# Performance work log

Measured on AMD Instinct MI355X. Metric: run time of the kernel, lower is better.

## Reference

```python
import jax, jax.numpy as jnp
import numpy as np

N, C, H, W = 32, 49, 9, 9   # batch, spectral bands (=outplane), spatial patch
MSIZE, K, PAD = 24, 7, 3    # conv3d out channels, spectral kernel, padding
EPS = 1e-5


def setup_inputs() -> dict:
    key = jax.random.key(0)
    k1, k2, k3 = jax.random.split(key, 3)
    x = jax.random.normal(k1, (N, C, H, W), dtype=jnp.float32)
    # Conv3d(1, MSIZE, [7,1,1]) params, PyTorch default uniform init
    fan_in = 1 * K * 1 * 1
    bound = 1.0 / np.sqrt(fan_in)
    conv_w = jax.random.uniform(k2, (MSIZE, 1, K, 1, 1), jnp.float32, -bound, bound)
    conv_b = jax.random.uniform(k3, (MSIZE,), jnp.float32, -bound, bound)
    # BatchNorm2d(49) affine params at init
    gamma = jnp.ones((C,), jnp.float32)
    beta = jnp.zeros((C,), jnp.float32)
    return {"x": x, "conv_w": conv_w, "conv_b": conv_b, "gamma": gamma, "beta": beta}


def reference(x, conv_w, conv_b, gamma, beta):
    n, c, h, w = x.shape
    # Conv3d over (depth=spectral, h, w) with kernel [K,1,1]: depth preserved
    x5 = x[:, None]  # (n,1,c,h,w)
    m = jax.lax.conv_general_dilated(
        x5, conv_w, window_strides=(1, 1, 1),
        padding=[(PAD, PAD), (0, 0), (0, 0)],
        dimension_numbers=("NCDHW", "OIDHW", "NCDHW"),
    ) + conv_b[None, :, None, None, None]        # (n, MSIZE, c, h, w)
    d = m.shape[1] * m.shape[2]                   # d = MSIZE * c
    mask = jax.nn.softmax(m.reshape(n, d, h * w), axis=-1).reshape(n, d, h, w)
    # original computes convm0 twice -> mask1 == mask0; reuse `mask` for both
    fk = jnp.einsum("ndhw,nchw->ncd", mask, x)    # (n, c, d)
    # out[n,c,h,w] = sum_d leaky_relu(fk[n,c,d] * mask[n,d,h,w])
    big = jnp.einsum("ncd,ndhw->ncdhw", fk, mask)  # (n,c,d,h,w) large intermediate
    out = jax.nn.leaky_relu(big, negative_slope=0.01).sum(axis=2)
    out = out + x                                  # residual
    # BatchNorm2d in training mode: batch statistics over (n,h,w) per channel
    mean = out.mean(axis=(0, 2, 3))
    var = out.var(axis=(0, 2, 3))
    out = (out - mean[:, None, None]) * jax.lax.rsqrt(var[:, None, None] + EPS)
    out = out * gamma[:, None, None] + beta[:, None, None]
    return out
```

## Files before the change

kernel.cpp:

```cpp
#include <hip/hip_runtime.h>
#include <hip/hip_bf16.h>

#define NN    32
#define CC    49
#define HWSZ  81
#define MSZ   24
#define KSZ   7
#define PADSZ 3
#define NHW   (NN*HWSZ)
#define NCHW  (NN*CC*HWSZ)

#define XSB_S  104
#define MSK_S  104
#define MSKT_S 72
#define G_S    72

typedef __attribute__((ext_vector_type(8))) short short8;
typedef __attribute__((ext_vector_type(4))) short short4v;
typedef __attribute__((ext_vector_type(4))) float f32x4;

__device__ __forceinline__ short f2b(float v) {
    unsigned u = __float_as_uint(v);
    u += 0x7fffu + ((u >> 16) & 1u);
    return (short)(u >> 16);
}
__device__ __forceinline__ float b2f(short s) {
    return __uint_as_float(((unsigned)(unsigned short)s) << 16);
}

__global__ __launch_bounds__(256) void fuse_k1(
    const float* __restrict__ x, const float* __restrict__ cw,
    const float* __restrict__ cb, float* __restrict__ acc, int use_ws)
{
    __shared__ short xsb [64 * XSB_S];
    __shared__ short msk [64 * MSK_S];
    __shared__ short mskT[96 * MSKT_S];
    __shared__ short gm  [64 * G_S];

    const int o = blockIdx.x;
    const int n = blockIdx.y;
    const int t = threadIdx.x;
    const int lane = t & 63;
    const int wv = t >> 6;
    const int lr = lane & 15;
    const int lq = lane >> 4;

    const float* xg = x + (size_t)n * CC * HWSZ;
    float wk[KSZ];
    #pragma unroll
    for (int k = 0; k < KSZ; ++k) wk[k] = cw[o * KSZ + k];
    const float bias = cb[o];

    const f32x4 z4 = {0.f, 0.f, 0.f, 0.f};
    for (int i = t; i < CC * HWSZ; i += 256) {
        int c = i / HWSZ, hw = i - c * HWSZ;
        xsb[c * XSB_S + hw] = f2b(xg[i]);
    }
    if (t < CC) {
        short* row = xsb + t * XSB_S;
        #pragma unroll
        for (int cq = 81; cq < 88; ++cq) row[cq] = 0;
        *(f32x4*)(row + 88) = z4;
        *(f32x4*)(row + 96) = z4;
    }
    for (int j = t; j < 15 * 13; j += 256) {
        int rr = j / 13, cg = j - rr * 13;
        *(f32x4*)(xsb + (49 + rr) * XSB_S + cg * 8) = z4;
    }
    for (int i = t; i < 832; i += 256) ((f32x4*)msk)[i] = z4;
    for (int i = t; i < 864; i += 256) ((f32x4*)mskT)[i] = z4;
    __syncthreads();

    #pragma unroll
    for (int it = 0; it < 4; ++it) {
        int dd = it * 16 + wv * 4 + lq;
        if (dd < CC) {
            float a0 = 0.f, a1 = 0.f, a2 = 0.f, a3 = 0.f, a4 = 0.f, a5 = 0.f;
            #pragma unroll
            for (int k = 0; k < KSZ; ++k) {
                int r = dd + k - PADSZ;
                if (r >= 0 && r < CC) {
                    const short* xr = xsb + r * XSB_S;
                    short4v xa = *(const short4v*)(xr + 4 * lr);
                    float w = wk[k];
                    a0 += w * b2f(xa[0]);
                    a1 += w * b2f(xa[1]);
                    a2 += w * b2f(xa[2]);
                    a3 += w * b2f(xa[3]);
                    a4 += w * b2f(xr[64 + lr]);
                    if (lr == 0) a5 += w * b2f(xr[80]);
                }
            }
            float e0 = __expf(a0 + bias), e1 = __expf(a1 + bias);
            float e2 = __expf(a2 + bias), e3 = __expf(a3 + bias);
            float e4 = __expf(a4 + bias);
            float e5 = (lr == 0) ? __expf(a5 + bias) : 0.f;
            float s = ((e0 + e1) + (e2 + e3)) + (e4 + e5);
            #pragma unroll
            for (int off = 8; off; off >>= 1) s += __shfl_xor(s, off, 64);
            float inv = __builtin_amdgcn_rcpf(s);
            short4v pk;
            pk[0] = f2b(e0 * inv); pk[1] = f2b(e1 * inv);
            pk[2] = f2b(e2 * inv); pk[3] = f2b(e3 * inv);
            short b4 = f2b(e4 * inv);
            short* mrow = msk + dd * MSK_S;
            *(short4v*)(mrow + 4 * lr) = pk;
            mrow[64 + lr] = b4;
            mskT[(4 * lr    ) * MSKT_S + dd] = pk[0];
            mskT[(4 * lr + 1) * MSKT_S + dd] = pk[1];
            mskT[(4 * lr + 2) * MSKT_S + dd] = pk[2];
            mskT[(4 * lr + 3) * MSKT_S + dd] = pk[3];
            mskT[(64 + lr   ) * MSKT_S + dd] = b4;
            if (lr == 0) {
                short b5 = f2b(e5 * inv);
                mrow[80] = b5;
                mskT[80 * MSKT_S + dd] = b5;
            }
        }
    }
    __syncthreads();

    {
        short8 a2[3];
        #pragma unroll
        for (int ks = 0; ks < 3; ++ks)
            a2[ks] = *(const short8*)&msk[(wv * 16 + lr) * MSK_S + ks * 32 + lq * 8];
        #pragma unroll
        for (int nt = 0; nt < 4; ++nt) {
            f32x4 accv = {0.f, 0.f, 0.f, 0.f};
            #pragma unroll
            for (int ks = 0; ks < 3; ++ks) {
                short8 b = *(const short8*)&xsb[(nt * 16 + lr) * XSB_S + ks * 32 + lq * 8];
                accv = __builtin_amdgcn_mfma_f32_16x16x32_bf16(a2[ks], b, accv, 0, 0, 0);
            }
            short4v pk;
            #pragma unroll
            for (int r = 0; r < 4; ++r) {
                float v = accv[r];
                v = (v >= 0.f) ? v : 0.01f * v;
                pk[r] = f2b(v);
            }
            *(short4v*)&gm[(nt * 16 + lr) * G_S + wv * 16 + lq * 4] = pk;
        }
    }
    __syncthreads();

    {
        short* bws = (short*)acc + (size_t)(o * NN + n) * CC * HWSZ;
        float* dstn = acc + (size_t)n * CC * HWSZ;
        short8 a1[2];
        #pragma unroll
        for (int ks = 0; ks < 2; ++ks)
            a1[ks] = *(const short8*)&gm[(wv * 16 + lr) * G_S + ks * 32 + lq * 8];
        #pragma unroll
        for (int nt = 0; nt < 6; ++nt) {
            f32x4 accv = {0.f, 0.f, 0.f, 0.f};
            #pragma unroll
            for (int ks = 0; ks < 2; ++ks) {
                short8 b = *(const short8*)&mskT[(nt * 16 + lr) * MSKT_S + ks * 32 + lq * 8];
                accv = __builtin_amdgcn_mfma_f32_16x16x32_bf16(a1[ks], b, accv, 0, 0, 0);
            }
            int hw = nt * 16 + lr;
            if (hw < HWSZ) {
                int cb = wv * 16 + lq * 4;
                if (use_ws) {
                    #pragma unroll
                    for (int r = 0; r < 4; ++r) {
                        int c = cb + r;
                        if (c < CC) bws[c * HWSZ + hw] = f2b(accv[r]);
                    }
                } else {
                    #pragma unroll
                    for (int r = 0; r < 4; ++r) {
                        int c = cb + r;
                        if (c < CC) atomicAdd(dstn + c * HWSZ + hw, accv[r]);
                    }
                }
            }
        }
    }
}

__global__ __launch_bounds__(1024) void fuse_k2w(
    const short* __restrict__ bws, const float* __restrict__ x,
    const float* __restrict__ gamma, const float* __restrict__ beta,
    float* __restrict__ out)
{
    const int c = blockIdx.x;
    const int t = threadIdx.x;
    float vals[3];
    float sum = 0.f, sq = 0.f;
    int cnt = 0;
    for (int i = t; i < NHW; i += 1024) {
        int n = i / HWSZ;
        int hw = i - n * HWSZ;
        int idx = (n * CC + c) * HWSZ + hw;
        const short* p = bws + idx;
        float v0 = x[idx], v1 = 0.f, v2 = 0.f, v3 = 0.f;
        #pragma unroll
        for (int o = 0; o < MSZ; o += 4) {
            v0 += b2f(p[(size_t)(o    ) * NCHW]);
            v1 += b2f(p[(size_t)(o + 1) * NCHW]);
            v2 += b2f(p[(size_t)(o + 2) * NCHW]);
            v3 += b2f(p[(size_t)(o + 3) * NCHW]);
        }
        float v = (v0 + v1) + (v2 + v3);
        vals[cnt++] = v;
        sum += v; sq += v * v;
    }
    #pragma unroll
    for (int off = 32; off; off >>= 1) {
        sum += __shfl_xor(sum, off, 64);
        sq  += __shfl_xor(sq, off, 64);
    }
    __shared__ float rs[16], rq[16];
    const int lane = t & 63, wv = t >> 6;
    if (lane == 0) { rs[wv] = sum; rq[wv] = sq; }
    __syncthreads();
    float ts = 0.f, tq = 0.f;
    #pragma unroll
    for (int w = 0; w < 16; ++w) { ts += rs[w]; tq += rq[w]; }
    const float invD = 1.f / (float)NHW;
    float mean = ts * invD;
    float var  = tq * invD - mean * mean;
    float scal = rsqrtf(var + 1e-5f) * gamma[c];
    float shft = beta[c] - mean * scal;
    cnt = 0;
    for (int i = t; i < NHW; i += 1024) {
        int n = i / HWSZ;
        int hw = i - n * HWSZ;
        out[(n * CC + c) * HWSZ + hw] = vals[cnt++] * scal + shft;
    }
}

__global__ __launch_bounds__(1024) void fuse_k2(
    float* __restrict__ out, const float* __restrict__ x,
    const float* __restrict__ gamma, const float* __restrict__ beta)
{
    const int c = blockIdx.x;
    const int t = threadIdx.x;
    float vals[3];
    float sum = 0.f, sq = 0.f;
    int cnt = 0;
    for (int i = t; i < NHW; i += 1024) {
        int n = i / HWSZ;
        int hw = i - n * HWSZ;
        int idx = (n * CC + c) * HWSZ + hw;
        float v = out[idx] + x[idx];
        vals[cnt++] = v;
        sum += v; sq += v * v;
    }
    #pragma unroll
    for (int off = 32; off; off >>= 1) {
        sum += __shfl_xor(sum, off, 64);
        sq  += __shfl_xor(sq, off, 64);
    }
    __shared__ float rs[16], rq[16];
    const int lane = t & 63, wv = t >> 6;
    if (lane == 0) { rs[wv] = sum; rq[wv] = sq; }
    __syncthreads();
    float ts = 0.f, tq = 0.f;
    #pragma unroll
    for (int w = 0; w < 16; ++w) { ts += rs[w]; tq += rq[w]; }
    const float invD = 1.f / (float)NHW;
    float mean = ts * invD;
    float var  = tq * invD - mean * mean;
    float scal = rsqrtf(var + 1e-5f) * gamma[c];
    float shft = beta[c] - mean * scal;
    cnt = 0;
    for (int i = t; i < NHW; i += 1024) {
        int n = i / HWSZ;
        int hw = i - n * HWSZ;
        out[(n * CC + c) * HWSZ + hw] = vals[cnt++] * scal + shft;
    }
}

extern "C" void kernel_launch(void* const* d_in, const int* in_sizes, int n_in,
                              void* d_out, int out_size, void* d_ws, size_t ws_size,
                              hipStream_t stream) {
    const float* x     = (const float*)d_in[0];
    const float* cw    = (const float*)d_in[1];
    const float* cb    = (const float*)d_in[2];
    const float* gamma = (const float*)d_in[3];
    const float* beta  = (const float*)d_in[4];
    float* out = (float*)d_out;

    const size_t need = (size_t)MSZ * NCHW * sizeof(short);
    if (ws_size >= need) {
        fuse_k1<<<dim3(MSZ, NN), 256, 0, stream>>>(x, cw, cb, (float*)d_ws, 1);
        fuse_k2w<<<CC, 1024, 0, stream>>>((const short*)d_ws, x, gamma, beta, out);
    } else {
        hipMemsetAsync(out, 0, (size_t)NCHW * sizeof(float), stream);
        fuse_k1<<<dim3(MSZ, NN), 256, 0, stream>>>(x, cw, cb, out, 0);
        fuse_k2<<<CC, 1024, 0, stream>>>(out, x, gamma, beta);
    }
}
```

Measured before the change: 79.96 us.

## Process three conv channels per block and accumulate in registers before atomics

Each block now handles three of the conv output channels with 512 threads. The output contributions are accumulated in MFMA registers across those channels, so each block issues one set of float atomics instead of one per channel. The bf16 workspace path and its reduction kernel are removed; the code always uses memset, atomics and the BN kernel. The intent is to cut the workspace write/read traffic, the number of atomics, and the repeated x staging per block. In exchange there are fewer blocks (8x32), an extra sync per channel iteration, and some atomic contention remains.

Measured after the change: 83.31 us. +4.2%, slower.

```diff
diff --git a/kernel.cpp b/kernel.cpp
--- a/kernel.cpp
+++ b/kernel.cpp
@@ -10,6 +10,9 @@
 #define NHW   (NN*HWSZ)
 #define NCHW  (NN*CC*HWSZ)
 
+#define OPB   3
+#define OGRP  (MSZ/OPB)
+
 #define XSB_S  104
 #define MSK_S  104
 #define MSKT_S 72
@@ -28,31 +31,27 @@
     return __uint_as_float(((unsigned)(unsigned short)s) << 16);
 }
 
-__global__ __launch_bounds__(256) void fuse_k1(
+__global__ __launch_bounds__(512) void fuse_k1(
     const float* __restrict__ x, const float* __restrict__ cw,
-    const float* __restrict__ cb, float* __restrict__ acc, int use_ws)
+    const float* __restrict__ cb, float* __restrict__ acc)
 {
     __shared__ short xsb [64 * XSB_S];
     __shared__ short msk [64 * MSK_S];
     __shared__ short mskT[96 * MSKT_S];
     __shared__ short gm  [64 * G_S];
 
-    const int o = blockIdx.x;
-    const int n = blockIdx.y;
-    const int t = threadIdx.x;
+    const int og = blockIdx.x;
+    const int n  = blockIdx.y;
+    const int t  = threadIdx.x;
     const int lane = t & 63;
     const int wv = t >> 6;
     const int lr = lane & 15;
     const int lq = lane >> 4;
 
     const float* xg = x + (size_t)n * CC * HWSZ;
-    float wk[KSZ];
-    #pragma unroll
-    for (int k = 0; k < KSZ; ++k) wk[k] = cw[o * KSZ + k];
-    const float bias = cb[o];
 
     const f32x4 z4 = {0.f, 0.f, 0.f, 0.f};
-    for (int i = t; i < CC * HWSZ; i += 256) {
+    for (int i = t; i < CC * HWSZ; i += 512) {
         int c = i / HWSZ, hw = i - c * HWSZ;
         xsb[c * XSB_S + hw] = f2b(xg[i]);
     }
@@ -63,173 +62,135 @@
         *(f32x4*)(row + 88) = z4;
         *(f32x4*)(row + 96) = z4;
     }
-    for (int j = t; j < 15 * 13; j += 256) {
+    for (int j = t; j < 15 * 13; j += 512) {
         int rr = j / 13, cg = j - rr * 13;
         *(f32x4*)(xsb + (49 + rr) * XSB_S + cg * 8) = z4;
     }
-    for (int i = t; i < 832; i += 256) ((f32x4*)msk)[i] = z4;
-    for (int i = t; i < 864; i += 256) ((f32x4*)mskT)[i] = z4;
+    for (int i = t; i < 832; i += 512) ((f32x4*)msk)[i] = z4;
+    for (int i = t; i < 864; i += 512) ((f32x4*)mskT)[i] = z4;
     __syncthreads();
 
-    #pragma unroll
-    for (int it = 0; it < 4; ++it) {
-        int dd = it * 16 + wv * 4 + lq;
-        if (dd < CC) {
-            float a0 = 0.f, a1 = 0.f, a2 = 0.f, a3 = 0.f, a4 = 0.f, a5 = 0.f;
-            #pragma unroll
-            for (int k = 0; k < KSZ; ++k) {
-                int r = dd + k - PADSZ;
-                if (r >= 0 && r < CC) {
-                    const short* xr = xsb + r * XSB_S;
-                    short4v xa = *(const short4v*)(xr + 4 * lr);
-                    float w = wk[k];
-                    a0 += w * b2f(xa[0]);
-                    a1 += w * b2f(xa[1]);
-                    a2 += w * b2f(xa[2]);
-                    a3 += w * b2f(xa[3]);
-                    a4 += w * b2f(xr[64 + lr]);
-                    if (lr == 0) a5 += w * b2f(xr[80]);
-                }
-            }
-            float e0 = __expf(a0 + bias), e1 = __expf(a1 + bias);
-            float e2 = __expf(a2 + bias), e3 = __expf(a3 + bias);
-            float e4 = __expf(a4 + bias);
-            float e5 = (lr == 0) ? __expf(a5 + bias) : 0.f;
-            float s = ((e0 + e1) + (e2 + e3)) + (e4 + e5);
-            #pragma unroll
-            for (int off = 8; off; off >>= 1) s += __shfl_xor(s, off, 64);
-            float inv = __builtin_amdgcn_rcpf(s);
-            short4v pk;
-            pk[0] = f2b(e0 * inv); pk[1] = f2b(e1 * inv);
-            pk[2] = f2b(e2 * inv); pk[3] = f2b(e3 * inv);
-            short b4 = f2b(e4 * inv);
-            short* mrow = msk + dd * MSK_S;
-            *(short4v*)(mrow + 4 * lr) = pk;
-            mrow[64 + lr] = b4;
-            mskT[(4 * lr    ) * MSKT_S + dd] = pk[0];
-            mskT[(4 * lr + 1) * MSKT_S + dd] = pk[1];
-            mskT[(4 * lr + 2) * MSKT_S + dd] = pk[2];
-            mskT[(4 * lr + 3) * MSKT_S + dd] = pk[3];
-            mskT[(64 + lr   ) * MSKT_S + dd] = b4;
-            if (lr == 0) {
-                short b5 = f2b(e5 * inv);
-                mrow[80] = b5;
-                mskT[80 * MSKT_S + dd] = b5;
-            }
-        }
-    }
-    __syncthreads();
-
-    {
-        short8 a2[3];
+    const int mt   = wv & 3;
+    const int ntc0 = (wv >> 2) * 2;
+    const int ct   = wv & 3;
+    const int nh   = (wv >> 2) * 3;
+
+    f32x4 dacc[3];
+    #pragma unroll
+    for (int j = 0; j < 3; ++j) dacc[j] = z4;
+
+    for (int oo = 0; oo < OPB; ++oo) {
+        const int o = og * OPB + oo;
+        float wk[KSZ];
         #pragma unroll
-        for (int ks = 0; ks < 3; ++ks)
-            a2[ks] = *(const short8*)&msk[(wv * 16 + lr) * MSK_S + ks * 32 + lq * 8];
+        for (int k = 0; k < KSZ; ++k) wk[k] = cw[o * KSZ + k];
+        const float bias = cb[o];
+
         #pragma unroll
-        for (int nt = 0; nt < 4; ++nt) {
-            f32x4 accv = {0.f, 0.f, 0.f, 0.f};
-            #pragma unroll
-            for (int ks = 0; ks < 3; ++ks) {
-                short8 b = *(const short8*)&xsb[(nt * 16 + lr) * XSB_S + ks * 32 + lq * 8];
-                accv = __builtin_amdgcn_mfma_f32_16x16x32_bf16(a2[ks], b, accv, 0, 0, 0);
-            }
-            short4v pk;
+        for (int it = 0; it < 2; ++it) {
+            int dd = it * 32 + wv * 4 + lq;
+            if (dd < CC) {
+                float a0 = 0.f, a1 = 0.f, a2 = 0.f, a3 = 0.f, a4 = 0.f, a5 = 0.f;
+                #pragma unroll
+                for (int k = 0; k < KSZ; ++k) {
+                    int r = dd + k - PADSZ;
+                    if (r >= 0 && r < CC) {
+                        const short* xr = xsb + r * XSB_S;
+                        short4v xa = *(const short4v*)(xr + 4 * lr);
+                        float w = wk[k];
+                        a0 += w * b2f(xa[0]);
+                        a1 += w * b2f(xa[1]);
+                        a2 += w * b2f(xa[2]);
+                        a3 += w * b2f(xa[3]);
+                        a4 += w * b2f(xr[64 + lr]);
+                        if (lr == 0) a5 += w * b2f(xr[80]);
+                    }
+                }
+                float e0 = __expf(a0 + bias), e1 = __expf(a1 + bias);
+                float e2 = __expf(a2 + bias), e3 = __expf(a3 + bias);
+                float e4 = __expf(a4 + bias);
+                float e5 = (lr == 0) ? __expf(a5 + bias) : 0.f;
+                float s = ((e0 + e1) + (e2 + e3)) + (e4 + e5);
+                #pragma unroll
+                for (int off = 8; off; off >>= 1) s += __shfl_xor(s, off, 64);
+                float inv = __builtin_amdgcn_rcpf(s);
+                short4v pk;
+                pk[0] = f2b(e0 * inv); pk[1] = f2b(e1 * inv);
+                pk[2] = f2b(e2 * inv); pk[3] = f2b(e3 * inv);
+                short b4 = f2b(e4 * inv);
+                short* mrow = msk + dd * MSK_S;
+                *(short4v*)(mrow + 4 * lr) = pk;
+                mrow[64 + lr] = b4;
+                mskT[(4 * lr    ) * MSKT_S + dd] = pk[0];
+                mskT[(4 * lr + 1) * MSKT_S + dd] = pk[1];
+                mskT[(4 * lr + 2) * MSKT_S + dd] = pk[2];
+                mskT[(4 * lr + 3) * MSKT_S + dd] = pk[3];
+                mskT[(64 + lr   ) * MSKT_S + dd] = b4;
+                if (lr == 0) {
+                    short b5 = f2b(e5 * inv);
+                    mrow[80] = b5;
+                    mskT[80 * MSKT_S + dd] = b5;
+                }
+            }
+        }
+        __syncthreads();
+
+        {
+            short8 a2f[3];
+            #pragma unroll
+            for (int ks = 0; ks < 3; ++ks)
+                a2f[ks] = *(const short8*)&msk[(mt * 16 + lr) * MSK_S + ks * 32 + lq * 8];
+            #pragma unroll
+            for (int jn = 0; jn < 2; ++jn) {
+                int nt = ntc0 + jn;
+                f32x4 accv = {0.f, 0.f, 0.f, 0.f};
+                #pragma unroll
+                for (int ks = 0; ks < 3; ++ks) {
+                    short8 b = *(const short8*)&xsb[(nt * 16 + lr) * XSB_S + ks * 32 + lq * 8];
+                    accv = __builtin_amdgcn_mfma_f32_16x16x32_bf16(a2f[ks], b, accv, 0, 0, 0);
+                }
+                short4v pk;
+                #pragma unroll
+                for (int r = 0; r < 4; ++r) {
+                    float v = accv[r];
+                    v = (v >= 0.f) ? v : 0.01f * v;
+                    pk[r] = f2b(v);
+                }
+                *(short4v*)&gm[(nt * 16 + lr) * G_S + mt * 16 + lq * 4] = pk;
+            }
+        }
+        __syncthreads();
+
+        {
+            short8 a1f[2];
+            #pragma unroll
+            for (int ks = 0; ks < 2; ++ks)
+                a1f[ks] = *(const short8*)&gm[(ct * 16 + lr) * G_S + ks * 32 + lq * 8];
+            #pragma unroll
+            for (int j = 0; j < 3; ++j) {
+                int nt = nh + j;
+                #pragma unroll
+                for (int ks = 0; ks < 2; ++ks) {
+                    short8 b = *(const short8*)&mskT[(nt * 16 + lr) * MSKT_S + ks * 32 + lq * 8];
+                    dacc[j] = __builtin_amdgcn_mfma_f32_16x16x32_bf16(a1f[ks], b, dacc[j], 0, 0, 0);
+                }
+            }
+        }
+        __syncthreads();
+    }
+
+    float* dstn = acc + (size_t)n * CC * HWSZ;
+    #pragma unroll
+    for (int j = 0; j < 3; ++j) {
+        int hw = (nh + j) * 16 + lr;
+        if (hw < HWSZ) {
+            int c0 = ct * 16 + lq * 4;
             #pragma unroll
             for (int r = 0; r < 4; ++r) {
-                float v = accv[r];
-                v = (v >= 0.f) ? v : 0.01f * v;
-                pk[r] = f2b(v);
-            }
-            *(short4v*)&gm[(nt * 16 + lr) * G_S + wv * 16 + lq * 4] = pk;
-        }
-    }
-    __syncthreads();
-
-    {
-        short* bws = (short*)acc + (size_t)(o * NN + n) * CC * HWSZ;
-        float* dstn = acc + (size_t)n * CC * HWSZ;
-        short8 a1[2];
-        #pragma unroll
-        for (int ks = 0; ks < 2; ++ks)
-            a1[ks] = *(const short8*)&gm[(wv * 16 + lr) * G_S + ks * 32 + lq * 8];
-        #pragma unroll
-        for (int nt = 0; nt < 6; ++nt) {
-            f32x4 accv = {0.f, 0.f, 0.f, 0.f};
-            #pragma unroll
-            for (int ks = 0; ks < 2; ++ks) {
-                short8 b = *(const short8*)&mskT[(nt * 16 + lr) * MSKT_S + ks * 32 + lq * 8];
-                accv = __builtin_amdgcn_mfma_f32_16x16x32_bf16(a1[ks], b, accv, 0, 0, 0);
-            }
-            int hw = nt * 16 + lr;
-            if (hw < HWSZ) {
-                int cb = wv * 16 + lq * 4;
-                if (use_ws) {
-                    #pragma unroll
-                    for (int r = 0; r < 4; ++r) {
-                        int c = cb + r;
-                        if (c < CC) bws[c * HWSZ + hw] = f2b(accv[r]);
-                    }
-                } else {
-                    #pragma unroll
-                    for (int r = 0; r < 4; ++r) {
-                        int c = cb + r;
-                        if (c < CC) atomicAdd(dstn + c * HWSZ + hw, accv[r]);
-                    }
-                }
-            }
-        }
-    }
-}
-
-__global__ __launch_bounds__(1024) void fuse_k2w(
-    const short* __restrict__ bws, const float* __restrict__ x,
-    const float* __restrict__ gamma, const float* __restrict__ beta,
-    float* __restrict__ out)
-{
-    const int c = blockIdx.x;
-    const int t = threadIdx.x;
-    float vals[3];
-    float sum = 0.f, sq = 0.f;
-    int cnt = 0;
-    for (int i = t; i < NHW; i += 1024) {
-        int n = i / HWSZ;
-        int hw = i - n * HWSZ;
-        int idx = (n * CC + c) * HWSZ + hw;
-        const short* p = bws + idx;
-        float v0 = x[idx], v1 = 0.f, v2 = 0.f, v3 = 0.f;
-        #pragma unroll
-        for (int o = 0; o < MSZ; o += 4) {
-            v0 += b2f(p[(size_t)(o    ) * NCHW]);
-            v1 += b2f(p[(size_t)(o + 1) * NCHW]);
-            v2 += b2f(p[(size_t)(o + 2) * NCHW]);
-            v3 += b2f(p[(size_t)(o + 3) * NCHW]);
-        }
-        float v = (v0 + v1) + (v2 + v3);
-        vals[cnt++] = v;
-        sum += v; sq += v * v;
-    }
-    #pragma unroll
-    for (int off = 32; off; off >>= 1) {
-        sum += __shfl_xor(sum, off, 64);
-        sq  += __shfl_xor(sq, off, 64);
-    }
-    __shared__ float rs[16], rq[16];
-    const int lane = t & 63, wv = t >> 6;
-    if (lane == 0) { rs[wv] = sum; rq[wv] = sq; }
-    __syncthreads();
-    float ts = 0.f, tq = 0.f;
-    #pragma unroll
-    for (int w = 0; w < 16; ++w) { ts += rs[w]; tq += rq[w]; }
-    const float invD = 1.f / (float)NHW;
-    float mean = ts * invD;
-    float var  = tq * invD - mean * mean;
-    float scal = rsqrtf(var + 1e-5f) * gamma[c];
-    float shft = beta[c] - mean * scal;
-    cnt = 0;
-    for (int i = t; i < NHW; i += 1024) {
-        int n = i / HWSZ;
-        int hw = i - n * HWSZ;
-        out[(n * CC + c) * HWSZ + hw] = vals[cnt++] * scal + shft;
+                int c = c0 + r;
+                if (c < CC) atomicAdd(dstn + c * HWSZ + hw, dacc[j][r]);
+            }
+        }
     }
 }
 
@@ -285,13 +246,7 @@
     const float* beta  = (const float*)d_in[4];
     float* out = (float*)d_out;
 
-    const size_t need = (size_t)MSZ * NCHW * sizeof(short);
-    if (ws_size >= need) {
-        fuse_k1<<<dim3(MSZ, NN), 256, 0, stream>>>(x, cw, cb, (float*)d_ws, 1);
-        fuse_k2w<<<CC, 1024, 0, stream>>>((const short*)d_ws, x, gamma, beta, out);
-    } else {
-        hipMemsetAsync(out, 0, (size_t)NCHW * sizeof(float), stream);
-        fuse_k1<<<dim3(MSZ, NN), 256, 0, stream>>>(x, cw, cb, out, 0);
-        fuse_k2<<<CC, 1024, 0, stream>>>(out, x, gamma, beta);
-    }
-}
+    hipMemsetAsync(out, 0, (size_t)NCHW * sizeof(float), stream);
+    fuse_k1<<<dim3(OGRP, NN), 512, 0, stream>>>(x, cw, cb, out);
+    fuse_k2<<<CC, 1024, 0, stream>>>(out, x, gamma, beta);
+}
```

## Split per-channel BatchNorm reduction into grouped partial-sum and normalize kernels

Applied to the files above, without the earlier changes.

The single 49-block batch-norm kernel (1024 threads per channel) becomes two kernels over a 49x8 grid. The first sums the 24 bf16 partial products plus the residual for a slice of the batch, writes the unnormalized output and stores per-group sum and sum-of-squares. The second combines the partial sums and normalizes in place. This spreads the strided workspace reads over many more blocks and CUs, at the cost of an extra kernel launch and an extra read and write of the output.

Result: no change. 80.95 us (+1.2%).

```diff
diff --git a/kernel.cpp b/kernel.cpp
--- a/kernel.cpp
+++ b/kernel.cpp
@@ -14,6 +14,10 @@
 #define MSK_S  104
 #define MSKT_S 72
 #define G_S    72
+
+#define NGRP  8
+#define NPG   (NN/NGRP)
+#define EPB   (NPG*HWSZ)
 
 typedef __attribute__((ext_vector_type(8))) short short8;
 typedef __attribute__((ext_vector_type(4))) short short4v;
@@ -181,20 +185,18 @@
     }
 }
 
-__global__ __launch_bounds__(1024) void fuse_k2w(
+__global__ __launch_bounds__(256) void fuse_k2a(
     const short* __restrict__ bws, const float* __restrict__ x,
-    const float* __restrict__ gamma, const float* __restrict__ beta,
-    float* __restrict__ out)
+    float* __restrict__ out, float2* __restrict__ psum)
 {
     const int c = blockIdx.x;
+    const int g = blockIdx.y;
     const int t = threadIdx.x;
-    float vals[3];
     float sum = 0.f, sq = 0.f;
-    int cnt = 0;
-    for (int i = t; i < NHW; i += 1024) {
-        int n = i / HWSZ;
-        int hw = i - n * HWSZ;
-        int idx = (n * CC + c) * HWSZ + hw;
+    for (int i = t; i < EPB; i += 256) {
+        int nl = i / HWSZ;
+        int hw = i - nl * HWSZ;
+        int idx = (((g * NPG + nl) * CC) + c) * HWSZ + hw;
         const short* p = bws + idx;
         float v0 = x[idx], v1 = 0.f, v2 = 0.f, v3 = 0.f;
         #pragma unroll
@@ -205,7 +207,7 @@
             v3 += b2f(p[(size_t)(o + 3) * NCHW]);
         }
         float v = (v0 + v1) + (v2 + v3);
-        vals[cnt++] = v;
+        out[idx] = v;
         sum += v; sq += v * v;
     }
     #pragma unroll
@@ -213,23 +215,41 @@
         sum += __shfl_xor(sum, off, 64);
         sq  += __shfl_xor(sq, off, 64);
     }
-    __shared__ float rs[16], rq[16];
+    __shared__ float rs[4], rq[4];
     const int lane = t & 63, wv = t >> 6;
     if (lane == 0) { rs[wv] = sum; rq[wv] = sq; }
     __syncthreads();
+    if (t == 0) {
+        float2 pv;
+        pv.x = (rs[0] + rs[1]) + (rs[2] + rs[3]);
+        pv.y = (rq[0] + rq[1]) + (rq[2] + rq[3]);
+        psum[c * NGRP + g] = pv;
+    }
+}
+
+__global__ __launch_bounds__(256) void fuse_k2b(
+    const float2* __restrict__ psum, const float* __restrict__ gamma,
+    const float* __restrict__ beta, float* __restrict__ out)
+{
+    const int c = blockIdx.x;
+    const int g = blockIdx.y;
+    const int t = threadIdx.x;
     float ts = 0.f, tq = 0.f;
     #pragma unroll
-    for (int w = 0; w < 16; ++w) { ts += rs[w]; tq += rq[w]; }
+    for (int w = 0; w < NGRP; ++w) {
+        float2 pv = psum[c * NGRP + w];
+        ts += pv.x; tq += pv.y;
+    }
     const float invD = 1.f / (float)NHW;
     float mean = ts * invD;
     float var  = tq * invD - mean * mean;
     float scal = rsqrtf(var + 1e-5f) * gamma[c];
     float shft = beta[c] - mean * scal;
-    cnt = 0;
-    for (int i = t; i < NHW; i += 1024) {
-        int n = i / HWSZ;
-        int hw = i - n * HWSZ;
-        out[(n * CC + c) * HWSZ + hw] = vals[cnt++] * scal + shft;
+    for (int i = t; i < EPB; i += 256) {
+        int nl = i / HWSZ;
+        int hw = i - nl * HWSZ;
+        int idx = (((g * NPG + nl) * CC) + c) * HWSZ + hw;
+        out[idx] = out[idx] * scal + shft;
     }
 }
 
@@ -285,10 +305,14 @@
     const float* beta  = (const float*)d_in[4];
     float* out = (float*)d_out;
 
-    const size_t need = (size_t)MSZ * NCHW * sizeof(short);
+    const size_t bws_bytes  = (size_t)MSZ * NCHW * sizeof(short);
+    const size_t psum_off   = bws_bytes;
+    const size_t need = psum_off + (size_t)CC * NGRP * sizeof(float2);
     if (ws_size >= need) {
+        float2* psum = (float2*)((char*)d_ws + psum_off);
         fuse_k1<<<dim3(MSZ, NN), 256, 0, stream>>>(x, cw, cb, (float*)d_ws, 1);
-        fuse_k2w<<<CC, 1024, 0, stream>>>((const short*)d_ws, x, gamma, beta, out);
+        fuse_k2a<<<dim3(CC, NGRP), 256, 0, stream>>>((const short*)d_ws, x, out, psum);
+        fuse_k2b<<<dim3(CC, NGRP), 256, 0, stream>>>(psum, gamma, beta, out);
     } else {
         hipMemsetAsync(out, 0, (size_t)NCHW * sizeof(float), stream);
         fuse_k1<<<dim3(MSZ, NN), 256, 0, stream>>>(x, cw, cb, out, 0);
```
